# Kernel tuning notes

Hardware: AMD Instinct MI355X
Metric: run time of the kernel (lower is better)

## Reference

```python
import jax, jax.numpy as jnp
import numpy as np

K, D = 8, 32          # num_heads, node_out_dim
KD = K * D            # 256
NEG = 0.2             # LeakyReLU negative slope
N, E = 100000, 300000
DIN, DREL = 128, 64


def setup_inputs() -> dict:
    key = jax.random.key(0)
    ks = iter(jax.random.split(key, 64))
    def nrm(shape, scale):
        return jax.random.normal(next(ks), shape, jnp.float32) * scale
    inp = {}
    # per-relation target-node features feats[(s,e,d)] : (N_d, d_in)
    for nm in ["feat_ui", "feat_iu", "feat_ii", "feat_ii_rev"]:
        inp[nm] = nrm((N, DIN), 1.0)
    # relation input features (d_rel,)
    for nm in ["r_ui", "r_iu", "r_ii", "r_ii_rev"]:
        inp[nm] = nrm((DREL,), 1.0)
    # fc_node per ntype (no bias), shared for src/dst roles
    inp["W_user"] = nrm((DIN, KD), 0.05)
    inp["W_item"] = nrm((DIN, KD), 0.05)
    # fc_rel per etype (no bias): d_rel -> 2*K*d
    for nm in ["Wrel_ui", "Wrel_iu", "Wrel_ii", "Wrel_ii_rev"]:
        inp[nm] = nrm((DREL, 2 * KD), 0.05)
    # cross-relation attention vectors (K, d)
    for nm in ["attn_ui", "attn_iu", "attn_ii", "attn_ii_rev"]:
        inp[nm] = nrm((K, D), 0.1)
    # residual fc per ntype (with bias) and residual gate scalar
    inp["Wres_user"] = nrm((DIN, KD), 0.05); inp["bres_user"] = nrm((KD,), 0.02)
    inp["Wres_item"] = nrm((DIN, KD), 0.05); inp["bres_item"] = nrm((KD,), 0.02)
    inp["a_user"] = jax.random.uniform(next(ks), (1,), jnp.float32)
    inp["a_item"] = jax.random.uniform(next(ks), (1,), jnp.float32)
    # fc_upd per etype (with bias): d_rel -> K*rel_out
    for nm in ["ui", "iu", "ii", "ii_rev"]:
        inp["Wupd_" + nm] = nrm((DREL, KD), 0.05)
        inp["bupd_" + nm] = nrm((KD,), 0.02)
    # edge lists per relation
    for nm in ["ui", "iu", "ii", "ii_rev"]:
        inp["src_" + nm] = jax.random.randint(next(ks), (E,), 0, N, jnp.int32)
        inp["dst_" + nm] = jax.random.randint(next(ks), (E,), 0, N, jnp.int32)
    return inp


def _conv(fsrc_in, fdst_in, Ws, Wd, Wrel, rfeat, src, dst):
    """RelationGraphConv: GAT-style attention over one bipartite relation."""
    n_dst = fdst_in.shape[0]
    fs = (fsrc_in @ Ws).reshape(-1, K, D)          # (Ns, K, D)
    fd = (fdst_in @ Wd).reshape(-1, K, D)          # (Nd, K, D)
    attn = (rfeat @ Wrel).reshape(K, 2 * D)        # (K, 2D)
    el = (fs * attn[:, :D]).sum(-1)                # (Ns, K)
    er = (fd * attn[:, D:]).sum(-1)                # (Nd, K)
    e = jax.nn.leaky_relu(el[src] + er[dst], NEG)  # (E, K)
    # edge softmax per destination node
    m = jax.ops.segment_max(e, dst, num_segments=n_dst)
    ex = jnp.exp(e - m[dst])
    s = jax.ops.segment_sum(ex, dst, num_segments=n_dst)
    a = ex / s[dst]                                # (E, K)
    msg = fs[src] * a[:, :, None]                  # (E, K, D)
    out = jax.ops.segment_sum(msg, dst, num_segments=n_dst)
    return jax.nn.relu(out.reshape(n_dst, KD))     # activation = relu


def _crossing(stacked, rel_attn):
    """RelationCrossing over stacked per-relation dst reps (R, N, K*D)."""
    R, Nn = stacked.shape[0], stacked.shape[1]
    f = stacked.reshape(R, Nn, K, D)
    sc = (rel_attn * f).sum(-1, keepdims=True)             # (R, N, K, 1)
    sc = jax.nn.softmax(jax.nn.leaky_relu(sc, NEG), axis=0)
    return (sc * f).sum(0).reshape(Nn, KD)


def reference(feat_ui, feat_iu, feat_ii, feat_ii_rev,
              r_ui, r_iu, r_ii, r_ii_rev,
              W_user, W_item,
              Wrel_ui, Wrel_iu, Wrel_ii, Wrel_ii_rev,
              attn_ui, attn_iu, attn_ii, attn_ii_rev,
              Wres_user, bres_user, Wres_item, bres_item,
              a_user, a_item,
              Wupd_ui, bupd_ui, Wupd_iu, bupd_iu,
              Wupd_ii, bupd_ii, Wupd_ii_rev, bupd_ii_rev,
              src_ui, dst_ui, src_iu, dst_iu,
              src_ii, dst_ii, src_ii_rev, dst_ii_rev):
    # relation convs; src feats come from the reverse relation's dict entry
    h_ui = _conv(feat_iu, feat_ui, W_user, W_item, Wrel_ui, r_ui, src_ui, dst_ui)
    h_iu = _conv(feat_ui, feat_iu, W_item, W_user, Wrel_iu, r_iu, src_iu, dst_iu)
    h_ii = _conv(feat_ii_rev, feat_ii, W_item, W_item, Wrel_ii, r_ii, src_ii, dst_ii)
    h_iir = _conv(feat_ii, feat_ii_rev, W_item, W_item, Wrel_ii_rev, r_ii_rev, src_ii_rev, dst_ii_rev)

    # gated residual per dtype
    def resid(h, fdst, Wres, bres, a):
        al = jax.nn.sigmoid(a)
        return al * h + (1.0 - al) * (fdst @ Wres + bres)

    h_ui = resid(h_ui, feat_ui, Wres_item, bres_item, a_item)
    h_iu = resid(h_iu, feat_iu, Wres_user, bres_user, a_user)
    h_ii = resid(h_ii, feat_ii, Wres_item, bres_item, a_item)
    h_iir = resid(h_iir, feat_ii_rev, Wres_item, bres_item, a_item)

    # cross-relation fusion: dtype item has relations [ui, ii, ii_rev]; user has [iu]
    item_stack = jnp.stack([h_ui, h_ii, h_iir], axis=0)
    out_ui = _crossing(item_stack, attn_ui)
    out_iu = h_iu  # num_rel == 1 -> identity
    out_ii = _crossing(item_stack, attn_ii)
    out_iir = _crossing(item_stack, attn_ii_rev)

    # relation feature update
    ro_ui = r_ui @ Wupd_ui + bupd_ui
    ro_iu = r_iu @ Wupd_iu + bupd_iu
    ro_ii = r_ii @ Wupd_ii + bupd_ii
    ro_iir = r_ii_rev @ Wupd_ii_rev + bupd_ii_rev
    return (out_ui, out_iu, out_ii, out_iir, ro_ui, ro_iu, ro_ii, ro_iir)
```

## Files before the change

kernel.cpp:

```cpp
#include <hip/hip_runtime.h>
#include <hip/hip_bf16.h>
#include <math.h>

#define NEG_SLOPE 0.2f
#define LOG2E 1.4426950408889634f

using bf16x8 = __attribute__((ext_vector_type(8))) short;
using f32x4  = __attribute__((ext_vector_type(4))) float;
using u16x8  = __attribute__((ext_vector_type(8))) unsigned short;
using u16x4  = __attribute__((ext_vector_type(4))) unsigned short;

__device__ __forceinline__ float lrelu(float x) { return x > 0.f ? x : NEG_SLOPE * x; }
__device__ __forceinline__ float dot4(float4 a, float4 b) {
    return a.x * b.x + a.y * b.y + a.z * b.z + a.w * b.w;
}
__device__ __forceinline__ unsigned short f2b(float x) {
    union { float f; unsigned u; } v; v.f = x;
    unsigned r = v.u + 0x7fff + ((v.u >> 16) & 1);
    return (unsigned short)(r >> 16);
}
__device__ __forceinline__ float b2f(unsigned short b) {
    union { unsigned u; float f; } v; v.u = ((unsigned)b) << 16;
    return v.f;
}
__device__ __forceinline__ float4 load4b(const unsigned short* p) {
    u16x4 u = *reinterpret_cast<const u16x4*>(p);
    return make_float4(b2f(u[0]), b2f(u[1]), b2f(u[2]), b2f(u[3]));
}
__device__ __forceinline__ bf16x8 cvt8(float4 a0, float4 a1) {
    union { u16x8 u; bf16x8 b; } c;
    c.u[0] = f2b(a0.x); c.u[1] = f2b(a0.y); c.u[2] = f2b(a0.z); c.u[3] = f2b(a0.w);
    c.u[4] = f2b(a1.x); c.u[5] = f2b(a1.y); c.u[6] = f2b(a1.z); c.u[7] = f2b(a1.w);
    return c.b;
}

struct PackArgs {
    const float* W1[4];
    const float* W2[4];
    const float* wvA[4];
    const float* wvB[4];
    unsigned short* Bp[4];
};

__global__ __launch_bounds__(256)
void pack_b_k(PackArgs pa)
{
    const int r = blockIdx.y;
    const int nb = blockIdx.x;
    const int ks = threadIdx.x >> 6;
    const int lane = threadIdx.x & 63;
    const int n = nb * 16 + (lane & 15);
    const int k0 = ks * 32 + (lane >> 4) * 8;
    u16x8 u;
    if (n < 512) {
        const float* Wsrc = (n < 256) ? (pa.W1[r] + n) : (pa.W2[r] + (n - 256));
        #pragma unroll
        for (int e = 0; e < 8; ++e) u[e] = f2b(Wsrc[(size_t)(k0 + e) * 256]);
    } else {
        const int h = (n - 512) & 7;
        const bool isEr = (n >= 520);
        const float* wv = isEr ? (pa.wvB[r] + h * 64 + 32) : (pa.wvA[r] + h * 64);
        const float* Wc = pa.W1[r] + h * 32;
        #pragma unroll
        for (int e = 0; e < 8; ++e) {
            const size_t k = (size_t)(k0 + e);
            float s = 0.f;
            #pragma unroll 8
            for (int d = 0; d < 32; ++d) s = fmaf(Wc[k * 256 + d], wv[d], s);
            u[e] = f2b(s);
        }
    }
    const size_t gid = (size_t)((nb * 4 + ks) * 64 + lane);
    *reinterpret_cast<u16x8*>(pa.Bp[r] + gid * 8) = u;
}

struct GemmArgs {
    const float* A[4];
    const unsigned short* Bp[4];
    const float* bres[4];
    unsigned short* pool[4];
    unsigned short* resid[4];
    float* elOut[4];
    float* erOut[4];
};

__global__ __launch_bounds__(256)
void mfma_gemm_k(GemmArgs ga, int Nrows)
{
    __shared__ __align__(16) char smem[32768];
    const int rsel = blockIdx.y;
    const int t = threadIdx.x;
    const int wv = t >> 6, lane = t & 63;
    const int l15 = lane & 15, lg = lane >> 4;
    const int nloc = wv * 16 + l15;
    const int m0 = blockIdx.x * 64;
    const int node = m0 + nloc;
    const bool valid = node < Nrows;
    const int nc = valid ? node : (Nrows - 1);

    const float* __restrict__ A = ga.A[rsel];
    const unsigned short* __restrict__ Bp = ga.Bp[rsel];
    const float* __restrict__ bres = ga.bres[rsel];

    bf16x8 bfr[4];
    #pragma unroll
    for (int ks = 0; ks < 4; ++ks) {
        const float* p = A + (size_t)nc * 128 + ks * 32 + lg * 8;
        float4 a0 = *reinterpret_cast<const float4*>(p);
        float4 a1 = *reinterpret_cast<const float4*>(p + 4);
        bfr[ks] = cvt8(a0, a1);
    }

    const int swz = (nloc & 7) << 4;
    u16x4 rh[16];

    #pragma unroll
    for (int i = 0; i < 16; ++i) {
        f32x4 accP = (f32x4){0.f, 0.f, 0.f, 0.f};
        f32x4 accR = (f32x4){0.f, 0.f, 0.f, 0.f};
        #pragma unroll
        for (int ks = 0; ks < 4; ++ks) {
            bf16x8 wfP = *reinterpret_cast<const bf16x8*>(
                Bp + ((size_t)((i * 4 + ks) * 64 + lane)) * 8);
            bf16x8 wfR = *reinterpret_cast<const bf16x8*>(
                Bp + ((size_t)(((i + 16) * 4 + ks) * 64 + lane)) * 8);
            accP = __builtin_amdgcn_mfma_f32_16x16x32_bf16(wfP, bfr[ks], accP, 0, 0, 0);
            accR = __builtin_amdgcn_mfma_f32_16x16x32_bf16(wfR, bfr[ks], accR, 0, 0, 0);
        }
        u16x4 o;
        o[0] = f2b(accP[0]); o[1] = f2b(accP[1]);
        o[2] = f2b(accP[2]); o[3] = f2b(accP[3]);
        const int byte = nloc * 512 + ((i * 32 + lg * 8) ^ swz);
        *reinterpret_cast<u16x4*>(smem + byte) = o;
        const int cb = i * 16 + lg * 4;
        float4 bv = *reinterpret_cast<const float4*>(bres + cb);
        rh[i][0] = f2b(accR[0] + bv.x); rh[i][1] = f2b(accR[1] + bv.y);
        rh[i][2] = f2b(accR[2] + bv.z); rh[i][3] = f2b(accR[3] + bv.w);
    }
    __syncthreads();
    {
        unsigned short* __restrict__ dst = ga.pool[rsel];
        #pragma unroll
        for (int i = 0; i < 8; ++i) {
            const int chunk = i * 256 + t;
            const int row = chunk >> 5;
            const int c16 = chunk & 31;
            const int byte = row * 512 + ((c16 * 16) ^ ((row & 7) << 4));
            u16x8 v = *reinterpret_cast<const u16x8*>(smem + byte);
            if (m0 + row < Nrows)
                *reinterpret_cast<u16x8*>(dst + (size_t)(m0 + row) * 256 + c16 * 8) = v;
        }
    }
    __syncthreads();
    #pragma unroll
    for (int i = 0; i < 16; ++i) {
        const int byte = nloc * 512 + ((i * 32 + lg * 8) ^ swz);
        *reinterpret_cast<u16x4*>(smem + byte) = rh[i];
    }
    __syncthreads();
    {
        unsigned short* __restrict__ dst = ga.resid[rsel];
        #pragma unroll
        for (int i = 0; i < 8; ++i) {
            const int chunk = i * 256 + t;
            const int row = chunk >> 5;
            const int c16 = chunk & 31;
            const int byte = row * 512 + ((c16 * 16) ^ ((row & 7) << 4));
            u16x8 v = *reinterpret_cast<const u16x8*>(smem + byte);
            if (m0 + row < Nrows)
                *reinterpret_cast<u16x8*>(dst + (size_t)(m0 + row) * 256 + c16 * 8) = v;
        }
    }

    {
        f32x4 acc = (f32x4){0.f, 0.f, 0.f, 0.f};
        #pragma unroll
        for (int ks = 0; ks < 4; ++ks) {
            bf16x8 wf = *reinterpret_cast<const bf16x8*>(
                Bp + ((size_t)((32 * 4 + ks) * 64 + lane)) * 8);
            acc = __builtin_amdgcn_mfma_f32_16x16x32_bf16(wf, bfr[ks], acc, 0, 0, 0);
        }
        if (valid) {
            float4 v = make_float4(acc[0], acc[1], acc[2], acc[3]);
            if (lg < 2)
                *reinterpret_cast<float4*>(ga.elOut[rsel] + (size_t)node * 8 + lg * 4) = v;
            else
                *reinterpret_cast<float4*>(ga.erOut[rsel] + (size_t)node * 8 + (lg - 2) * 4) = v;
        }
    }
}

struct EdgePtrs {
    const int* src[4];
    const int* dst[4];
    int E[4];
    int csrOff[4];
};

__global__ __launch_bounds__(256)
void hist_k(EdgePtrs ep, int* __restrict__ counts4, int N)
{
    const int r = blockIdx.y;
    const int e = blockIdx.x * 256 + threadIdx.x;
    if (e < ep.E[r]) atomicAdd(counts4 + (size_t)r * N + ep.dst[r][e], 1);
}

__global__ __launch_bounds__(256)
void blksum_k(const int* __restrict__ counts4, int* __restrict__ blksum4, int N)
{
    const int r = blockIdx.y;
    const int* c = counts4 + (size_t)r * N;
    const int base = blockIdx.x * 1024 + threadIdx.x;
    int s = 0;
    #pragma unroll
    for (int i = 0; i < 4; ++i) { int idx = base + i * 256; if (idx < N) s += c[idx]; }
    __shared__ int sd[256];
    sd[threadIdx.x] = s; __syncthreads();
    for (int off = 128; off > 0; off >>= 1) {
        if (threadIdx.x < off) sd[threadIdx.x] += sd[threadIdx.x + off];
        __syncthreads();
    }
    if (threadIdx.x == 0) blksum4[r * 1024 + blockIdx.x] = sd[0];
}

__global__ __launch_bounds__(1024)
void scanblk_k(int* __restrict__ blksum4, int nbx)
{
    const int r = blockIdx.x;
    const int t = threadIdx.x;
    __shared__ int sd[1024];
    int v = (t < nbx) ? blksum4[r * 1024 + t] : 0;
    sd[t] = v; __syncthreads();
    for (int off = 1; off < 1024; off <<= 1) {
        int u = (t >= off) ? sd[t - off] : 0;
        __syncthreads();
        sd[t] += u;
        __syncthreads();
    }
    if (t < nbx) blksum4[r * 1024 + t] = sd[t] - v;
}

__global__ __launch_bounds__(256)
void cursor_k(const int* __restrict__ counts4, const int* __restrict__ blkoff4,
              int* __restrict__ cursor4, int N)
{
    const int r = blockIdx.y;
    const int* c = counts4 + (size_t)r * N;
    int* cur = cursor4 + (size_t)r * N;
    const int t = threadIdx.x;
    const int base = blockIdx.x * 1024 + t * 4;
    const int c0 = (base + 0 < N) ? c[base + 0] : 0;
    const int c1 = (base + 1 < N) ? c[base + 1] : 0;
    const int c2 = (base + 2 < N) ? c[base + 2] : 0;
    const int c3 = (base + 3 < N) ? c[base + 3] : 0;
    const int tsum = c0 + c1 + c2 + c3;
    __shared__ int sd[256];
    sd[t] = tsum; __syncthreads();
    for (int off = 1; off < 256; off <<= 1) {
        int u = (t >= off) ? sd[t - off] : 0;
        __syncthreads();
        sd[t] += u;
        __syncthreads();
    }
    int excl = sd[t] - tsum + blkoff4[r * 1024 + blockIdx.x];
    if (base + 0 < N) cur[base + 0] = excl;
    if (base + 1 < N) cur[base + 1] = excl + c0;
    if (base + 2 < N) cur[base + 2] = excl + c0 + c1;
    if (base + 3 < N) cur[base + 3] = excl + c0 + c1 + c2;
}

__global__ __launch_bounds__(256)
void scatter_k(EdgePtrs ep, int* __restrict__ cursor4, int* __restrict__ csr_src, int N)
{
    const int r = blockIdx.y;
    const int e = blockIdx.x * 256 + threadIdx.x;
    if (e < ep.E[r]) {
        const int d = ep.dst[r][e];
        const int pos = atomicAdd(cursor4 + (size_t)r * N + d, 1);
        csr_src[ep.csrOff[r] + pos] = ep.src[r][e];
    }
}

struct NodeArgs {
    const int* csr[4];
    const int* cursor[4];
    const int* counts[4];
    const float* el[4];
    const float* er[4];
    const unsigned short* pool[4];
    const unsigned short* resid[4];
};

__global__ __launch_bounds__(256)
void node_k(NodeArgs na,
            const float* __restrict__ attn_ui, const float* __restrict__ attn_ii,
            const float* __restrict__ attn_iir,
            const float* __restrict__ a_user, const float* __restrict__ a_item,
            float* __restrict__ out, int Nrows)
{
    const int lane = threadIdx.x & 63;
    const int n = blockIdx.x * 4 + (threadIdx.x >> 6);
    if (n >= Nrows) return;
    const int k = lane >> 3;

    int deg[4], endv[4];
    float erk[4];
    #pragma unroll
    for (int r = 0; r < 4; ++r) {
        deg[r]  = na.counts[r][n];
        endv[r] = na.cursor[r][n];
        erk[r]  = na.er[r][(size_t)n * 8 + k];
    }

    const float si = 1.f / (1.f + __expf(-a_item[0])), osi = 1.f - si;
    const float su = 1.f / (1.f + __expf(-a_user[0])), osu = 1.f - su;

    float4 fr[4];
    #pragma unroll
    for (int r = 0; r < 4; ++r) {
        const int d = deg[r];
        const int start = endv[r] - d;
        const int* __restrict__ csr = na.csr[r];
        const float* __restrict__ elr = na.el[r];
        const unsigned short* __restrict__ fs = na.pool[r];
        const float er_k = erk[r];
        float s = 0.f;
        float4 acc = make_float4(0.f, 0.f, 0.f, 0.f);
        for (int base = 0; base < d; base += 4) {
            const int m = d - base;
            int sidx[4];
            #pragma unroll
            for (int u = 0; u < 4; ++u)
                sidx[u] = csr[start + base + ((u < m) ? u : 0)];
            float ex[4];
            #pragma unroll
            for (int u = 0; u < 4; ++u) {
                const float x = elr[(size_t)sidx[u] * 8 + k] + er_k;
                const float e = __builtin_amdgcn_exp2f(fmaxf(x, NEG_SLOPE * x));
                ex[u] = (u < m) ? e : 0.f;
            }
            float4 pv[4];
            #pragma unroll
            for (int u = 0; u < 4; ++u)
                pv[u] = load4b(fs + (size_t)sidx[u] * 256 + lane * 4);
            #pragma unroll
            for (int u = 0; u < 4; ++u) {
                s += ex[u];
                acc.x = fmaf(pv[u].x, ex[u], acc.x);
                acc.y = fmaf(pv[u].y, ex[u], acc.y);
                acc.z = fmaf(pv[u].z, ex[u], acc.z);
                acc.w = fmaf(pv[u].w, ex[u], acc.w);
            }
        }
        const float inv = (d > 0) ? 1.f / s : 0.f;
        float4 R = load4b(na.resid[r] + (size_t)n * 256 + lane * 4);
        const float sg = (r == 1) ? su : si;
        const float og = (r == 1) ? osu : osi;
        fr[r].x = sg * fmaxf(acc.x * inv, 0.f) + og * R.x;
        fr[r].y = sg * fmaxf(acc.y * inv, 0.f) + og * R.y;
        fr[r].z = sg * fmaxf(acc.z * inv, 0.f) + og * R.z;
        fr[r].w = sg * fmaxf(acc.w * inv, 0.f) + og * R.w;
    }

    const float4 f0 = fr[0], f1 = fr[2], f2 = fr[3], fiu = fr[1];
    float4 w0 = *reinterpret_cast<const float4*>(attn_ui  + lane * 4);
    float4 w1 = *reinterpret_cast<const float4*>(attn_ii  + lane * 4);
    float4 w2 = *reinterpret_cast<const float4*>(attn_iir + lane * 4);

    float p[3][3];
    p[0][0] = dot4(w0, f0); p[0][1] = dot4(w0, f1); p[0][2] = dot4(w0, f2);
    p[1][0] = dot4(w1, f0); p[1][1] = dot4(w1, f1); p[1][2] = dot4(w1, f2);
    p[2][0] = dot4(w2, f0); p[2][1] = dot4(w2, f1); p[2][2] = dot4(w2, f2);
    #pragma unroll
    for (int x = 0; x < 3; ++x)
        #pragma unroll
        for (int r = 0; r < 3; ++r)
            #pragma unroll
            for (int m = 1; m < 8; m <<= 1)
                p[x][r] += __shfl_xor(p[x][r], m, 64);

    const size_t NK = (size_t)Nrows * 256;
    const size_t o = (size_t)n * 256 + lane * 4;
    const size_t xoff[3] = {0, 2 * NK, 3 * NK};
    #pragma unroll
    for (int x = 0; x < 3; ++x) {
        float a0 = lrelu(p[x][0]), a1 = lrelu(p[x][1]), a2 = lrelu(p[x][2]);
        float mx = fmaxf(a0, fmaxf(a1, a2));
        float e0 = __expf(a0 - mx), e1 = __expf(a1 - mx), e2 = __expf(a2 - mx);
        float inv = 1.f / (e0 + e1 + e2);
        e0 *= inv; e1 *= inv; e2 *= inv;
        float4 rr;
        rr.x = e0 * f0.x + e1 * f1.x + e2 * f2.x;
        rr.y = e0 * f0.y + e1 * f1.y + e2 * f2.y;
        rr.z = e0 * f0.z + e1 * f1.z + e2 * f2.z;
        rr.w = e0 * f0.w + e1 * f1.w + e2 * f2.w;
        *reinterpret_cast<float4*>(out + xoff[x] + o) = rr;
    }
    *reinterpret_cast<float4*>(out + NK + o) = fiu;
}

struct RelPtrs {
    const float* rf[4];
    const float* Wrel[4];
    const float* Wupd[4];
    const float* bupd[4];
};

__global__ __launch_bounds__(512)
void rel_k(RelPtrs P, float* __restrict__ wvec, float* __restrict__ ro)
{
    const int r = blockIdx.x;
    const int t = threadIdx.x;
    __shared__ float rfs[64];
    if (t < 64) rfs[t] = P.rf[r][t];
    __syncthreads();
    {
        const float* Wc = P.Wrel[r];
        float acc = 0.f;
        #pragma unroll 8
        for (int i = 0; i < 64; ++i) acc = fmaf(rfs[i], Wc[(size_t)i * 512 + t], acc);
        wvec[(size_t)r * 512 + t] = acc * LOG2E;
    }
    if (t < 256) {
        const float* Wc = P.Wupd[r];
        float acc = P.bupd[r][t];
        #pragma unroll 8
        for (int i = 0; i < 64; ++i) acc = fmaf(rfs[i], Wc[(size_t)i * 256 + t], acc);
        ro[(size_t)r * 256 + t] = acc;
    }
}

extern "C" void kernel_launch(void* const* d_in, const int* in_sizes, int n_in,
                              void* d_out, int out_size, void* d_ws, size_t ws_size,
                              hipStream_t stream)
{
    (void)n_in; (void)out_size; (void)ws_size;
    const float* feat_ui  = (const float*)d_in[0];
    const float* feat_iu  = (const float*)d_in[1];
    const float* feat_ii  = (const float*)d_in[2];
    const float* feat_iir = (const float*)d_in[3];
    const float* W_user   = (const float*)d_in[8];
    const float* W_item   = (const float*)d_in[9];
    const float* Wres_user = (const float*)d_in[18];
    const float* bres_user = (const float*)d_in[19];
    const float* Wres_item = (const float*)d_in[20];
    const float* bres_item = (const float*)d_in[21];
    const float* a_user = (const float*)d_in[22];
    const float* a_item = (const float*)d_in[23];
    const int N = in_sizes[0] / 128;
    const int Es[4] = {in_sizes[32], in_sizes[34], in_sizes[36], in_sizes[38]};
    int maxE = 0;
    for (int r = 0; r < 4; ++r) maxE = Es[r] > maxE ? Es[r] : maxE;

    const size_t NP = (size_t)N * 256;
    const size_t N8 = (size_t)N * 8;
    const size_t BPSZ = 33 * 4 * 64 * 8;

    unsigned short* us = (unsigned short*)d_ws;
    unsigned short* pool[4];
    unsigned short* resid[4];
    for (int r = 0; r < 4; ++r) pool[r]  = us + (size_t)r * NP;
    for (int r = 0; r < 4; ++r) resid[r] = us + (size_t)(4 + r) * NP;
    unsigned short* BpArr[4];
    for (int r = 0; r < 4; ++r) BpArr[r] = us + 8 * NP + (size_t)r * BPSZ;
    float* fl = (float*)(us + 8 * NP + 4 * BPSZ);
    float *el[4], *er[4];
    for (int r = 0; r < 4; ++r) { el[r] = fl + (size_t)(2 * r) * N8; er[r] = fl + (size_t)(2 * r + 1) * N8; }
    float* wvec = fl + 8 * N8;
    int* counts4 = (int*)(wvec + 4 * 512);
    int* cursor4 = counts4 + 4 * (size_t)N;
    int* blksum4 = cursor4 + 4 * (size_t)N;
    int* csr_src = blksum4 + 4 * 1024;
    float* out = (float*)d_out;

    EdgePtrs ep;
    {
        int off = 0;
        const int si[4] = {32, 34, 36, 38};
        for (int r = 0; r < 4; ++r) {
            ep.src[r] = (const int*)d_in[si[r]];
            ep.dst[r] = (const int*)d_in[si[r] + 1];
            ep.E[r] = Es[r];
            ep.csrOff[r] = off;
            off += Es[r];
        }
    }

    (void)hipMemsetAsync(counts4, 0, 4 * (size_t)N * sizeof(int), stream);

    RelPtrs rp;
    rp.rf[0]   = (const float*)d_in[4];  rp.rf[1]   = (const float*)d_in[5];
    rp.rf[2]   = (const float*)d_in[6];  rp.rf[3]   = (const float*)d_in[7];
    rp.Wrel[0] = (const float*)d_in[10]; rp.Wrel[1] = (const float*)d_in[11];
    rp.Wrel[2] = (const float*)d_in[12]; rp.Wrel[3] = (const float*)d_in[13];
    rp.Wupd[0] = (const float*)d_in[24]; rp.Wupd[1] = (const float*)d_in[26];
    rp.Wupd[2] = (const float*)d_in[28]; rp.Wupd[3] = (const float*)d_in[30];
    rp.bupd[0] = (const float*)d_in[25]; rp.bupd[1] = (const float*)d_in[27];
    rp.bupd[2] = (const float*)d_in[29]; rp.bupd[3] = (const float*)d_in[31];
    rel_k<<<dim3(4), dim3(512), 0, stream>>>(rp, wvec, out + 4 * NP);

    const int pair[4] = {1, 0, 3, 2};
    PackArgs pa;
    pa.W1[0] = W_user; pa.W2[0] = Wres_user;
    pa.W1[1] = W_item; pa.W2[1] = Wres_item;
    pa.W1[2] = W_item; pa.W2[2] = Wres_item;
    pa.W1[3] = W_item; pa.W2[3] = Wres_item;
    for (int r = 0; r < 4; ++r) {
        pa.wvA[r] = wvec + (size_t)r * 512;
        pa.wvB[r] = wvec + (size_t)pair[r] * 512;
        pa.Bp[r]  = BpArr[r];
    }
    pack_b_k<<<dim3(33, 4), 256, 0, stream>>>(pa);

    const int geb = (maxE + 255) / 256;
    const int nbx = (N + 1023) / 1024;
    hist_k<<<dim3(geb, 4), 256, 0, stream>>>(ep, counts4, N);
    blksum_k<<<dim3(nbx, 4), 256, 0, stream>>>(counts4, blksum4, N);
    scanblk_k<<<dim3(4), 1024, 0, stream>>>(blksum4, nbx);
    cursor_k<<<dim3(nbx, 4), 256, 0, stream>>>(counts4, blksum4, cursor4, N);
    scatter_k<<<dim3(geb, 4), 256, 0, stream>>>(ep, cursor4, csr_src, N);

    GemmArgs ga;
    ga.A[0] = feat_iu;  ga.bres[0] = bres_user;
    ga.A[1] = feat_ui;  ga.bres[1] = bres_item;
    ga.A[2] = feat_iir; ga.bres[2] = bres_item;
    ga.A[3] = feat_ii;  ga.bres[3] = bres_item;
    for (int r = 0; r < 4; ++r) {
        ga.Bp[r]    = BpArr[r];
        ga.pool[r]  = pool[r];
        ga.resid[r] = resid[pair[r]];
        ga.elOut[r] = el[r];
        ga.erOut[r] = er[pair[r]];
    }
    const int gb = (N + 63) / 64;
    mfma_gemm_k<<<dim3(gb, 4), 256, 0, stream>>>(ga, N);

    NodeArgs na;
    for (int r = 0; r < 4; ++r) {
        na.csr[r]    = csr_src + ep.csrOff[r];
        na.cursor[r] = cursor4 + (size_t)r * N;
        na.counts[r] = counts4 + (size_t)r * N;
        na.el[r]     = el[r];
        na.er[r]     = er[r];
        na.pool[r]   = pool[r];
        na.resid[r]  = resid[r];
    }
    const int nb4 = (N + 3) / 4;
    node_k<<<nb4, 256, 0, stream>>>(na,
                                    (const float*)d_in[14], (const float*)d_in[16],
                                    (const float*)d_in[17],
                                    a_user, a_item, out, N);
}
```

Baseline: 642.4 us.

## Reuse weight fragments across two row groups in GEMM; shuffle-share edge exps

The GEMM kernel drops to 128 threads per block, and each wave now computes two 16-row groups, so every loaded weight fragment feeds two MFMAs. The projection and residual passes are split into separate loops, which frees the rh register array. In node_k, each lane computes one exp for one (edge, head) pair and the four per-edge values are gathered with shuffles, replacing redundant el loads and exps across the 8 lanes of a head. Fewer waves per block and higher register use per thread may lower occupancy.

```diff
diff --git a/kernel.cpp b/kernel.cpp
--- a/kernel.cpp
+++ b/kernel.cpp
@@ -84,7 +84,7 @@
     float* erOut[4];
 };
 
-__global__ __launch_bounds__(256)
+__global__ __launch_bounds__(128)
 void mfma_gemm_k(GemmArgs ga, int Nrows)
 {
     __shared__ __align__(16) char smem[32768];
@@ -92,57 +92,54 @@
     const int t = threadIdx.x;
     const int wv = t >> 6, lane = t & 63;
     const int l15 = lane & 15, lg = lane >> 4;
-    const int nloc = wv * 16 + l15;
     const int m0 = blockIdx.x * 64;
-    const int node = m0 + nloc;
-    const bool valid = node < Nrows;
-    const int nc = valid ? node : (Nrows - 1);
 
     const float* __restrict__ A = ga.A[rsel];
     const unsigned short* __restrict__ Bp = ga.Bp[rsel];
     const float* __restrict__ bres = ga.bres[rsel];
 
-    bf16x8 bfr[4];
-    #pragma unroll
-    for (int ks = 0; ks < 4; ++ks) {
-        const float* p = A + (size_t)nc * 128 + ks * 32 + lg * 8;
-        float4 a0 = *reinterpret_cast<const float4*>(p);
-        float4 a1 = *reinterpret_cast<const float4*>(p + 4);
-        bfr[ks] = cvt8(a0, a1);
-    }
-
-    const int swz = (nloc & 7) << 4;
-    u16x4 rh[16];
+    int nloc[2], swzg[2], nodeg[2];
+    bool validg[2];
+    bf16x8 bfr[2][4];
+    #pragma unroll
+    for (int g = 0; g < 2; ++g) {
+        nloc[g] = wv * 32 + g * 16 + l15;
+        swzg[g] = (nloc[g] & 7) << 4;
+        nodeg[g] = m0 + nloc[g];
+        validg[g] = nodeg[g] < Nrows;
+        const int nc = validg[g] ? nodeg[g] : (Nrows - 1);
+        #pragma unroll
+        for (int ks = 0; ks < 4; ++ks) {
+            const float* p = A + (size_t)nc * 128 + ks * 32 + lg * 8;
+            float4 a0 = *reinterpret_cast<const float4*>(p);
+            float4 a1 = *reinterpret_cast<const float4*>(p + 4);
+            bfr[g][ks] = cvt8(a0, a1);
+        }
+    }
 
     #pragma unroll
     for (int i = 0; i < 16; ++i) {
-        f32x4 accP = (f32x4){0.f, 0.f, 0.f, 0.f};
-        f32x4 accR = (f32x4){0.f, 0.f, 0.f, 0.f};
+        f32x4 acc0 = (f32x4){0.f, 0.f, 0.f, 0.f};
+        f32x4 acc1 = (f32x4){0.f, 0.f, 0.f, 0.f};
         #pragma unroll
         for (int ks = 0; ks < 4; ++ks) {
-            bf16x8 wfP = *reinterpret_cast<const bf16x8*>(
+            bf16x8 wf = *reinterpret_cast<const bf16x8*>(
                 Bp + ((size_t)((i * 4 + ks) * 64 + lane)) * 8);
-            bf16x8 wfR = *reinterpret_cast<const bf16x8*>(
-                Bp + ((size_t)(((i + 16) * 4 + ks) * 64 + lane)) * 8);
-            accP = __builtin_amdgcn_mfma_f32_16x16x32_bf16(wfP, bfr[ks], accP, 0, 0, 0);
-            accR = __builtin_amdgcn_mfma_f32_16x16x32_bf16(wfR, bfr[ks], accR, 0, 0, 0);
-        }
-        u16x4 o;
-        o[0] = f2b(accP[0]); o[1] = f2b(accP[1]);
-        o[2] = f2b(accP[2]); o[3] = f2b(accP[3]);
-        const int byte = nloc * 512 + ((i * 32 + lg * 8) ^ swz);
-        *reinterpret_cast<u16x4*>(smem + byte) = o;
-        const int cb = i * 16 + lg * 4;
-        float4 bv = *reinterpret_cast<const float4*>(bres + cb);
-        rh[i][0] = f2b(accR[0] + bv.x); rh[i][1] = f2b(accR[1] + bv.y);
-        rh[i][2] = f2b(accR[2] + bv.z); rh[i][3] = f2b(accR[3] + bv.w);
+            acc0 = __builtin_amdgcn_mfma_f32_16x16x32_bf16(wf, bfr[0][ks], acc0, 0, 0, 0);
+            acc1 = __builtin_amdgcn_mfma_f32_16x16x32_bf16(wf, bfr[1][ks], acc1, 0, 0, 0);
+        }
+        u16x4 o0, o1;
+        o0[0] = f2b(acc0[0]); o0[1] = f2b(acc0[1]); o0[2] = f2b(acc0[2]); o0[3] = f2b(acc0[3]);
+        o1[0] = f2b(acc1[0]); o1[1] = f2b(acc1[1]); o1[2] = f2b(acc1[2]); o1[3] = f2b(acc1[3]);
+        *reinterpret_cast<u16x4*>(smem + nloc[0] * 512 + ((i * 32 + lg * 8) ^ swzg[0])) = o0;
+        *reinterpret_cast<u16x4*>(smem + nloc[1] * 512 + ((i * 32 + lg * 8) ^ swzg[1])) = o1;
     }
     __syncthreads();
     {
         unsigned short* __restrict__ dst = ga.pool[rsel];
         #pragma unroll
-        for (int i = 0; i < 8; ++i) {
-            const int chunk = i * 256 + t;
+        for (int i = 0; i < 16; ++i) {
+            const int chunk = i * 128 + t;
             const int row = chunk >> 5;
             const int c16 = chunk & 31;
             const int byte = row * 512 + ((c16 * 16) ^ ((row & 7) << 4));
@@ -152,17 +149,34 @@
         }
     }
     __syncthreads();
+
     #pragma unroll
     for (int i = 0; i < 16; ++i) {
-        const int byte = nloc * 512 + ((i * 32 + lg * 8) ^ swz);
-        *reinterpret_cast<u16x4*>(smem + byte) = rh[i];
+        f32x4 acc0 = (f32x4){0.f, 0.f, 0.f, 0.f};
+        f32x4 acc1 = (f32x4){0.f, 0.f, 0.f, 0.f};
+        #pragma unroll
+        for (int ks = 0; ks < 4; ++ks) {
+            bf16x8 wf = *reinterpret_cast<const bf16x8*>(
+                Bp + ((size_t)(((i + 16) * 4 + ks) * 64 + lane)) * 8);
+            acc0 = __builtin_amdgcn_mfma_f32_16x16x32_bf16(wf, bfr[0][ks], acc0, 0, 0, 0);
+            acc1 = __builtin_amdgcn_mfma_f32_16x16x32_bf16(wf, bfr[1][ks], acc1, 0, 0, 0);
+        }
+        const int cb = i * 16 + lg * 4;
+        float4 bv = *reinterpret_cast<const float4*>(bres + cb);
+        u16x4 o0, o1;
+        o0[0] = f2b(acc0[0] + bv.x); o0[1] = f2b(acc0[1] + bv.y);
+        o0[2] = f2b(acc0[2] + bv.z); o0[3] = f2b(acc0[3] + bv.w);
+        o1[0] = f2b(acc1[0] + bv.x); o1[1] = f2b(acc1[1] + bv.y);
+        o1[2] = f2b(acc1[2] + bv.z); o1[3] = f2b(acc1[3] + bv.w);
+        *reinterpret_cast<u16x4*>(smem + nloc[0] * 512 + ((i * 32 + lg * 8) ^ swzg[0])) = o0;
+        *reinterpret_cast<u16x4*>(smem + nloc[1] * 512 + ((i * 32 + lg * 8) ^ swzg[1])) = o1;
     }
     __syncthreads();
     {
         unsigned short* __restrict__ dst = ga.resid[rsel];
         #pragma unroll
-        for (int i = 0; i < 8; ++i) {
-            const int chunk = i * 256 + t;
+        for (int i = 0; i < 16; ++i) {
+            const int chunk = i * 128 + t;
             const int row = chunk >> 5;
             const int c16 = chunk & 31;
             const int byte = row * 512 + ((c16 * 16) ^ ((row & 7) << 4));
@@ -173,19 +187,24 @@
     }
 
     {
-        f32x4 acc = (f32x4){0.f, 0.f, 0.f, 0.f};
+        f32x4 acc0 = (f32x4){0.f, 0.f, 0.f, 0.f};
+        f32x4 acc1 = (f32x4){0.f, 0.f, 0.f, 0.f};
         #pragma unroll
         for (int ks = 0; ks < 4; ++ks) {
             bf16x8 wf = *reinterpret_cast<const bf16x8*>(
                 Bp + ((size_t)((32 * 4 + ks) * 64 + lane)) * 8);
-            acc = __builtin_amdgcn_mfma_f32_16x16x32_bf16(wf, bfr[ks], acc, 0, 0, 0);
-        }
-        if (valid) {
-            float4 v = make_float4(acc[0], acc[1], acc[2], acc[3]);
+            acc0 = __builtin_amdgcn_mfma_f32_16x16x32_bf16(wf, bfr[0][ks], acc0, 0, 0, 0);
+            acc1 = __builtin_amdgcn_mfma_f32_16x16x32_bf16(wf, bfr[1][ks], acc1, 0, 0, 0);
+        }
+        #pragma unroll
+        for (int g = 0; g < 2; ++g) {
+            if (!validg[g]) continue;
+            f32x4 a = g ? acc1 : acc0;
+            float4 v = make_float4(a[0], a[1], a[2], a[3]);
             if (lg < 2)
-                *reinterpret_cast<float4*>(ga.elOut[rsel] + (size_t)node * 8 + lg * 4) = v;
+                *reinterpret_cast<float4*>(ga.elOut[rsel] + (size_t)nodeg[g] * 8 + lg * 4) = v;
             else
-                *reinterpret_cast<float4*>(ga.erOut[rsel] + (size_t)node * 8 + (lg - 2) * 4) = v;
+                *reinterpret_cast<float4*>(ga.erOut[rsel] + (size_t)nodeg[g] * 8 + (lg - 2) * 4) = v;
         }
     }
 }
@@ -301,15 +320,17 @@
     const int lane = threadIdx.x & 63;
     const int n = blockIdx.x * 4 + (threadIdx.x >> 6);
     if (n >= Nrows) return;
-    const int k = lane >> 3;
+    const int khead = lane >> 3;
+    const int h = lane & 7;
+    const int usel = khead & 3;
 
     int deg[4], endv[4];
-    float erk[4];
+    float erh[4];
     #pragma unroll
     for (int r = 0; r < 4; ++r) {
         deg[r]  = na.counts[r][n];
         endv[r] = na.cursor[r][n];
-        erk[r]  = na.er[r][(size_t)n * 8 + k];
+        erh[r]  = na.er[r][(size_t)n * 8 + h];
     }
 
     const float si = 1.f / (1.f + __expf(-a_item[0])), osi = 1.f - si;
@@ -323,7 +344,7 @@
         const int* __restrict__ csr = na.csr[r];
         const float* __restrict__ elr = na.el[r];
         const unsigned short* __restrict__ fs = na.pool[r];
-        const float er_k = erk[r];
+        const float er_h = erh[r];
         float s = 0.f;
         float4 acc = make_float4(0.f, 0.f, 0.f, 0.f);
         for (int base = 0; base < d; base += 4) {
@@ -332,12 +353,13 @@
             #pragma unroll
             for (int u = 0; u < 4; ++u)
                 sidx[u] = csr[start + base + ((u < m) ? u : 0)];
+            const float x = elr[(size_t)sidx[usel] * 8 + h] + er_h;
+            const float e1 = __builtin_amdgcn_exp2f(fmaxf(x, NEG_SLOPE * x));
             float ex[4];
             #pragma unroll
             for (int u = 0; u < 4; ++u) {
-                const float x = elr[(size_t)sidx[u] * 8 + k] + er_k;
-                const float e = __builtin_amdgcn_exp2f(fmaxf(x, NEG_SLOPE * x));
-                ex[u] = (u < m) ? e : 0.f;
+                float ev = __shfl(e1, u * 8 + khead, 64);
+                ex[u] = (u < m) ? ev : 0.f;
             }
             float4 pv[4];
             #pragma unroll
@@ -533,7 +555,7 @@
         ga.erOut[r] = er[pair[r]];
     }
     const int gb = (N + 63) / 64;
-    mfma_gemm_k<<<dim3(gb, 4), 256, 0, stream>>>(ga, N);
+    mfma_gemm_k<<<dim3(gb, 4), 128, 0, stream>>>(ga, N);
 
     NodeArgs na;
     for (int r = 0; r < 4; ++r) {
```

Result: slower. 659.6 us (+2.7%).
